# Optimization experiments

Measured on AMD Instinct MI355X. Metric: run time of the kernel, lower is better.

Reference implementation:

```python
import jax, jax.numpy as jnp
import numpy as np

N_NODES = 80000
N_EDGES = 1280000
D_NODE = 128
D_EDGE = 32
HID = 64
OUT = 32
EPS_GEN = 1e-7
EPS_BN = 1e-5


def _lin_init(key, fan_in, fan_out):
    return (jax.random.normal(key, (fan_in, fan_out), jnp.float32) / np.sqrt(fan_in))


def setup_inputs() -> dict:
    key = jax.random.key(0)
    ks = jax.random.split(key, 20)
    inp = {
        "x": jax.random.normal(ks[0], (N_NODES, D_NODE), jnp.float32),
        "edge_index": jax.random.randint(ks[1], (2, N_EDGES), 0, N_NODES, jnp.int32),
        "edge_attr": jax.random.normal(ks[2], (N_EDGES, D_EDGE), jnp.float32),
        # encoders
        "node_W": _lin_init(ks[3], D_NODE, HID), "node_b": jnp.zeros((HID,), jnp.float32),
        "edge_W": _lin_init(ks[4], D_EDGE, HID), "edge_b": jnp.zeros((HID,), jnp.float32),
        # GENConv layer 1 MLP: [HID -> 2HID (bias=False)] -> BN -> ReLU -> [2HID -> HID (bias=False)]
        "c1_W1": _lin_init(ks[5], HID, 2 * HID), "c1_g": jnp.ones((2 * HID,), jnp.float32), "c1_be": jnp.zeros((2 * HID,), jnp.float32), "c1_W2": _lin_init(ks[6], 2 * HID, HID),
        # GENConv layer 2
        "c2_W1": _lin_init(ks[7], HID, 2 * HID), "c2_g": jnp.ones((2 * HID,), jnp.float32), "c2_be": jnp.zeros((2 * HID,), jnp.float32), "c2_W2": _lin_init(ks[8], 2 * HID, HID),
        # edge update linears on concat(3*HID)
        "l1_W": _lin_init(ks[9], 3 * HID, HID), "l1_b": jnp.zeros((HID,), jnp.float32),
        "l2_W": _lin_init(ks[10], 3 * HID, OUT), "l2_b": jnp.zeros((OUT,), jnp.float32),
    }
    return inp


def _scatter_softmax_agg(msg, dst, n_nodes):
    # SoftmaxAggregation with t=1: per-destination, per-feature softmax weights
    m = jax.ops.segment_max(msg, dst, num_segments=n_nodes)  # [N, H]
    m = jnp.where(jnp.isfinite(m), m, 0.0)                   # nodes w/o in-edges
    ex = jnp.exp(msg - m[dst])                               # [E, H]
    denom = jax.ops.segment_sum(ex, dst, num_segments=n_nodes)
    alpha = ex / (denom[dst] + 1e-16)
    return jax.ops.segment_sum(msg * alpha, dst, num_segments=n_nodes)


def _batchnorm(h, gamma, beta):
    mu = jnp.mean(h, axis=0)
    var = jnp.var(h, axis=0)
    return (h - mu) * jax.lax.rsqrt(var + EPS_BN) * gamma + beta


def _genconv(x, src, dst, edge_attr, W1, g, be, W2):
    msg = jax.nn.relu(x[src] + edge_attr) + EPS_GEN          # [E, HID]
    agg = _scatter_softmax_agg(msg, dst, x.shape[0])         # [N, HID]
    h = agg + x
    h = jax.nn.relu(_batchnorm(h @ W1, g, be))
    return h @ W2


def reference(x, edge_index, edge_attr, node_W, node_b, edge_W, edge_b,
              c1_W1, c1_g, c1_be, c1_W2, c2_W1, c2_g, c2_be, c2_W2,
              l1_W, l1_b, l2_W, l2_b):
    src, dst = edge_index[0], edge_index[1]
    ea = edge_attr @ edge_W + edge_b                          # [E, HID]
    h = x @ node_W + node_b                                   # [N, HID]

    convs = [(c1_W1, c1_g, c1_be, c1_W2), (c2_W1, c2_g, c2_be, c2_W2)]
    lins = [(l1_W, l1_b), (l2_W, l2_b)]
    for (W1, g, be, W2), (lW, lb) in zip(convs, lins):
        h = jax.nn.relu(_genconv(h, src, dst, ea, W1, g, be, W2))
        # dropout is identity in eval mode
        ef = jnp.concatenate([h[src], ea, h[dst]], axis=-1)   # [E, 3*HID]
        ea = ef @ lW + lb
    return h, ea
```

## Files before the change

### kernel.cpp

```cpp
#include <hip/hip_runtime.h>
#include <hip/hip_bf16.h>

#define N_NODES 80000
#define N_EDGES 1280000
constexpr int DN = 128;
constexpr int DE = 32;
constexpr int H  = 64;
constexpr int H2 = 128;
constexpr int CSTRIDE = 32;
constexpr float EPS_GEN = 1e-7f;
constexpr float EPS_BN  = 1e-5f;

typedef _Float16 f16x8 __attribute__((ext_vector_type(8)));
typedef _Float16 f16x4 __attribute__((ext_vector_type(4)));
typedef float f32x4 __attribute__((ext_vector_type(4)));

__device__ __forceinline__ void atomAddF(float* p, float v) {
  __hip_atomic_fetch_add(p, v, __ATOMIC_RELAXED, __HIP_MEMORY_SCOPE_AGENT);
}

struct PrepDesc { const float* W; _Float16* img; int K; int OC; int blkStart; };
struct PrepAll { PrepDesc d[8]; };

__global__ void k_prep_all(PrepAll P) {
  int b = blockIdx.x;
  int i = 0;
#pragma unroll
  for (int t = 1; t < 8; ++t)
    if (P.d[t].blkStart <= b) i = t;
  const PrepDesc D = P.d[i];
  int idx = (b - D.blkStart) * 256 + threadIdx.x;
  if (idx >= D.K * D.OC) return;
  int nslabK = D.K >> 5;
  int j = idx & 7, m16 = (idx >> 3) & 15, kg = (idx >> 7) & 3;
  int slab = idx >> 9;
  int kk = slab % nslabK, n2 = slab / nslabK;
  int k = kk * 32 + kg * 8 + j, n = n2 * 16 + m16;
  D.img[idx] = (_Float16)D.W[k * D.OC + n];
}

template <int K, int OC, bool IN16, bool BIAS,
          bool RELU_OUT, bool OUT16, bool OUT32, bool SCATOUT, bool STATS>
__global__ __launch_bounds__(256) void k_dense(
    const void* __restrict__ Ain, const _Float16* __restrict__ wimg,
    const float* __restrict__ bias,
    const int* __restrict__ posmap,
    _Float16* __restrict__ out16, float* __restrict__ out32,
    float* __restrict__ sums_out) {
  constexpr int NK = K / 32, NF = OC / 16;
  __shared__ float sStat[STATS ? 1024 : 1];
  const int tid = threadIdx.x, wv = tid >> 6, lane = tid & 63;
  const int m16 = lane & 15, kg = lane >> 4;
  const int rowbase = blockIdx.x * 64 + wv * 16;
  const int arow = rowbase + m16;
  f32x4 acc[NF];
#pragma unroll
  for (int n2 = 0; n2 < NF; ++n2) {
    float bv = BIAS ? bias[n2 * 16 + m16] : 0.0f;
    acc[n2] = (f32x4){bv, bv, bv, bv};
  }
  const _Float16* wp = wimg + (size_t)lane * 8;
#pragma unroll
  for (int kk = 0; kk < NK; ++kk) {
    f16x8 a;
    if constexpr (IN16) {
      const _Float16* ap = (const _Float16*)Ain + (size_t)arow * K + kg * 8 + kk * 32;
      a = *(const f16x8*)ap;
    } else {
      const float* ap = (const float*)Ain + (size_t)arow * K + kg * 8 + kk * 32;
      float4 v0 = *(const float4*)ap;
      float4 v1 = *(const float4*)(ap + 4);
      a = (f16x8){(_Float16)v0.x, (_Float16)v0.y, (_Float16)v0.z, (_Float16)v0.w,
                  (_Float16)v1.x, (_Float16)v1.y, (_Float16)v1.z, (_Float16)v1.w};
    }
#pragma unroll
    for (int n2 = 0; n2 < NF; ++n2) {
      f16x8 bb = *(const f16x8*)(wp + ((size_t)(n2 * NK + kk) << 9));
      acc[n2] = __builtin_amdgcn_mfma_f32_16x16x32_f16(a, bb, acc[n2], 0, 0, 0);
    }
  }
  if constexpr (OUT16 || OUT32) {
#pragma unroll
    for (int n2 = 0; n2 < NF; ++n2)
#pragma unroll
      for (int r = 0; r < 4; ++r) {
        float o = acc[n2][r];
        if constexpr (RELU_OUT) o = fmaxf(o, 0.0f);
        int orow = rowbase + kg * 4 + r;
        if constexpr (SCATOUT) orow = posmap[orow];
        size_t oi = (size_t)orow * OC + n2 * 16 + m16;
        if constexpr (OUT16) out16[oi] = (_Float16)o;
        if constexpr (OUT32) out32[oi] = o;
      }
  }
  if constexpr (STATS) {
    static_assert(!STATS || NF == 8, "STATS assumes OC==128");
#pragma unroll
    for (int n2 = 0; n2 < NF; ++n2) {
      float s = acc[n2][0] + acc[n2][1] + acc[n2][2] + acc[n2][3];
      float q = acc[n2][0] * acc[n2][0] + acc[n2][1] * acc[n2][1] +
                acc[n2][2] * acc[n2][2] + acc[n2][3] * acc[n2][3];
      s += __shfl_xor(s, 16); s += __shfl_xor(s, 32);
      q += __shfl_xor(q, 16); q += __shfl_xor(q, 32);
      if (kg == 0) {
        sStat[wv * 128 + n2 * 16 + m16] = s;
        sStat[512 + wv * 128 + n2 * 16 + m16] = q;
      }
    }
    __syncthreads();
    {
      int which = tid >> 7, f = tid & 127;
      const float* b0 = sStat + which * 512;
      float v = b0[f] + b0[128 + f] + b0[256 + f] + b0[384 + f];
      atomAddF(&sums_out[which * H2 + f], v);
    }
  }
}

template <bool OUT32>
__global__ __launch_bounds__(256) void k_mlp2f(
    const _Float16* __restrict__ hsum, const _Float16* __restrict__ w1img,
    const _Float16* __restrict__ w2img, const float* __restrict__ sums,
    const float* __restrict__ g, const float* __restrict__ be,
    _Float16* __restrict__ out16, float* __restrict__ out32) {
  constexpr int TP = 136;
  __shared__ float sSC[H2], sSH[H2];
  __shared__ _Float16 sT[64 * TP];
  const int tid = threadIdx.x, wv = tid >> 6, lane = tid & 63;
  const int m16 = lane & 15, kg = lane >> 4;
  const int rowbase = blockIdx.x * 64 + wv * 16;

  for (int i = tid; i < H2; i += 256) {
    float mu  = sums[i] * (1.0f / N_NODES);
    float var = sums[H2 + i] * (1.0f / N_NODES) - mu * mu;
    float sc  = rsqrtf(var + EPS_BN) * g[i];
    sSC[i] = sc;
    sSH[i] = be[i] - mu * sc;
  }

  f32x4 acc1[8];
#pragma unroll
  for (int n2 = 0; n2 < 8; ++n2) acc1[n2] = (f32x4){0.f, 0.f, 0.f, 0.f};
  const _Float16* wp1 = w1img + (size_t)lane * 8;
#pragma unroll
  for (int kk = 0; kk < 2; ++kk) {
    f16x8 a = *(const f16x8*)(hsum + (size_t)(rowbase + m16) * H + kg * 8 + kk * 32);
#pragma unroll
    for (int n2 = 0; n2 < 8; ++n2) {
      f16x8 bb = *(const f16x8*)(wp1 + ((size_t)(n2 * 2 + kk) << 9));
      acc1[n2] = __builtin_amdgcn_mfma_f32_16x16x32_f16(a, bb, acc1[n2], 0, 0, 0);
    }
  }
  __syncthreads();
#pragma unroll
  for (int n2 = 0; n2 < 8; ++n2) {
    int col = n2 * 16 + m16;
    float sc = sSC[col], sh = sSH[col];
#pragma unroll
    for (int r = 0; r < 4; ++r) {
      float v = fmaxf(fmaf(acc1[n2][r], sc, sh), 0.0f);
      sT[(wv * 16 + kg * 4 + r) * TP + col] = (_Float16)v;
    }
  }
  __syncthreads();
  f32x4 acc2[4];
#pragma unroll
  for (int n2 = 0; n2 < 4; ++n2) acc2[n2] = (f32x4){0.f, 0.f, 0.f, 0.f};
  const _Float16* wp2 = w2img + (size_t)lane * 8;
#pragma unroll
  for (int kk = 0; kk < 4; ++kk) {
    f16x8 a2 = *(const f16x8*)&sT[(wv * 16 + m16) * TP + kg * 8 + kk * 32];
#pragma unroll
    for (int n2 = 0; n2 < 4; ++n2) {
      f16x8 bb = *(const f16x8*)(wp2 + ((size_t)(n2 * 4 + kk) << 9));
      acc2[n2] = __builtin_amdgcn_mfma_f32_16x16x32_f16(a2, bb, acc2[n2], 0, 0, 0);
    }
  }
#pragma unroll
  for (int n2 = 0; n2 < 4; ++n2)
#pragma unroll
    for (int r = 0; r < 4; ++r) {
      float o = fmaxf(acc2[n2][r], 0.0f);
      size_t oi = (size_t)(rowbase + kg * 4 + r) * H + n2 * 16 + m16;
      out16[oi] = (_Float16)o;
      if constexpr (OUT32) out32[oi] = o;
    }
}

template <int OC, typename OUT_T, int T, bool SCAT>
__global__ __launch_bounds__(256) void k_edge_upd_srt(
    const _Float16* __restrict__ h, const _Float16* __restrict__ ea,
    const int4* __restrict__ eidsQ,
    const _Float16* __restrict__ wimg, const float* __restrict__ lb,
    OUT_T* __restrict__ eout) {
  constexpr int NF = OC / 16;
  __shared__ _Float16 sWf[NF * 6 * 512];
  __shared__ int sS[T * 64], sD[T * 64];
  __shared__ int sE[SCAT ? T * 64 : 1];
  const int tid = threadIdx.x, wv = tid >> 6, lane = tid & 63;
  const int m16 = lane & 15, kg = lane >> 4;
  const int p0 = blockIdx.x * (T * 64);

  for (int i = tid; i < T * 64; i += 256) {
    int4 t = eidsQ[p0 + i];
    sS[i] = t.y;
    sD[i] = t.z;
    if constexpr (SCAT) sE[i] = t.x;
  }
  {
    const float4* s4 = (const float4*)wimg;
    float4* d4 = (float4*)sWf;
    constexpr int NV = NF * 6 * 512 / 8;
    for (int i = tid; i < NV; i += 256) d4[i] = s4[i];
  }
  __syncthreads();
  const _Float16* wp = sWf + (size_t)lane * 8;

  float bias_[NF];
#pragma unroll
  for (int n2 = 0; n2 < NF; ++n2) bias_[n2] = lb[n2 * 16 + m16];

  f16x8 FA[6], FB[6];
  auto LOADA = [&](f16x8* F, int l) {
    const _Float16* a0 = h + (size_t)sS[l] * H + kg * 8;
    const _Float16* a1 = ea + (size_t)(p0 + l) * H + kg * 8;
    const _Float16* a2 = h + (size_t)sD[l] * H + kg * 8;
    F[0] = *(const f16x8*)a0;
    F[1] = *(const f16x8*)(a0 + 32);
    F[2] = *(const f16x8*)a1;
    F[3] = *(const f16x8*)(a1 + 32);
    F[4] = *(const f16x8*)a2;
    F[5] = *(const f16x8*)(a2 + 32);
  };
  auto COMPUTE = [&](const f16x8* F, int l) {
    f32x4 acc[NF];
#pragma unroll
    for (int n2 = 0; n2 < NF; ++n2)
      acc[n2] = (f32x4){bias_[n2], bias_[n2], bias_[n2], bias_[n2]};
#pragma unroll
    for (int kk = 0; kk < 6; ++kk)
#pragma unroll
      for (int n2 = 0; n2 < NF; ++n2) {
        f16x8 bb = *(const f16x8*)(wp + ((n2 * 6 + kk) << 9));
        acc[n2] = __builtin_amdgcn_mfma_f32_16x16x32_f16(F[kk], bb, acc[n2], 0, 0, 0);
      }
    const int lbase = l - m16;
#pragma unroll
    for (int n2 = 0; n2 < NF; ++n2)
#pragma unroll
      for (int r = 0; r < 4; ++r) {
        int lr = lbase + kg * 4 + r;
        int col = n2 * 16 + m16;
        if constexpr (SCAT)
          eout[(size_t)sE[lr] * OC + col] = (OUT_T)acc[n2][r];
        else
          eout[(size_t)(p0 + lr) * OC + col] = (OUT_T)acc[n2][r];
      }
  };

  const int l0 = wv * 16 + m16;
  LOADA(FA, l0);
  if (T > 1) LOADA(FB, l0 + 64);
#pragma unroll
  for (int t = 0; t < T; ++t) {
    if (t & 1) {
      COMPUTE(FB, l0 + t * 64);
      if (t + 2 < T) LOADA(FB, l0 + (t + 2) * 64);
    } else {
      COMPUTE(FA, l0 + t * 64);
      if (t + 2 < T) LOADA(FA, l0 + (t + 2) * 64);
    }
  }
}

__global__ void k_rank(const int* __restrict__ dst, int* cntPad, int* __restrict__ rank) {
  int e = blockIdx.x * blockDim.x + threadIdx.x;
  if (e < N_EDGES)
    rank[e] = atomicAdd(&cntPad[(size_t)dst[e] * CSTRIDE], 1);
}

__global__ void k_scan_blk(const int* __restrict__ cntPad, int* __restrict__ bsum) {
  __shared__ int sh[256];
  int i = blockIdx.x * 256 + threadIdx.x;
  sh[threadIdx.x] = (i < N_NODES) ? cntPad[(size_t)i * CSTRIDE] : 0;
  __syncthreads();
  for (int s = 128; s > 0; s >>= 1) {
    if (threadIdx.x < s) sh[threadIdx.x] += sh[threadIdx.x + s];
    __syncthreads();
  }
  if (threadIdx.x == 0) bsum[blockIdx.x] = sh[0];
}

__global__ void k_scan_top(int* bsum, int nb) {
  __shared__ int sh[512];
  int t = threadIdx.x;
  int orig = (t < nb) ? bsum[t] : 0;
  sh[t] = orig;
  __syncthreads();
  for (int off = 1; off < 512; off <<= 1) {
    int v = (t >= off) ? sh[t - off] : 0;
    __syncthreads();
    sh[t] += v;
    __syncthreads();
  }
  if (t < nb) bsum[t] = sh[t] - orig;
}

__global__ void k_scan_fin(const int* __restrict__ cntPad, const int* __restrict__ bsum,
                           int* __restrict__ start, int* __restrict__ cntC) {
  __shared__ int sh[256];
  int i = blockIdx.x * 256 + threadIdx.x;
  int t = threadIdx.x;
  int orig = (i < N_NODES) ? cntPad[(size_t)i * CSTRIDE] : 0;
  sh[t] = orig;
  __syncthreads();
  for (int off = 1; off < 256; off <<= 1) {
    int v = (t >= off) ? sh[t - off] : 0;
    __syncthreads();
    sh[t] += v;
    __syncthreads();
  }
  if (i < N_NODES) {
    start[i] = bsum[blockIdx.x] + sh[t] - orig;
    cntC[i] = orig;
  }
}

__global__ void k_scatter(const int* __restrict__ src, const int* __restrict__ dst,
                          const int* __restrict__ rank, const int* __restrict__ start,
                          int4* __restrict__ eidsQ, int* __restrict__ posOf) {
  int e = blockIdx.x * blockDim.x + threadIdx.x;
  if (e < N_EDGES) {
    int d = dst[e];
    int pos = start[d] + rank[e];
    eidsQ[pos] = make_int4(e, src[e], d, 0);
    posOf[e] = pos;
  }
}

__global__ __launch_bounds__(256) void k_agg_csr(
    const _Float16* __restrict__ h, const _Float16* __restrict__ ea_s,
    const int4* __restrict__ eidsQ, const int* __restrict__ start,
    const int* __restrict__ cnt, _Float16* __restrict__ hsum,
    float* __restrict__ sums_clr) {
  if (blockIdx.x == 0) sums_clr[threadIdx.x] = 0.0f;
  const int lane = threadIdx.x & 63;
  const int wid  = (int)((blockIdx.x * blockDim.x + threadIdx.x) >> 6);
  if (wid >= N_NODES) return;
  const int ep = lane >> 3, fg = lane & 7;
  const int s0 = start[wid], c = cnt[wid];
  float num[8] = {0.f, 0.f, 0.f, 0.f, 0.f, 0.f, 0.f, 0.f};
  float den[8] = {0.f, 0.f, 0.f, 0.f, 0.f, 0.f, 0.f, 0.f};
  if (c > 0) {
    const int nit = (c + 7) >> 3;
    int idx = min(ep, c - 1);
    int2 pe = *(const int2*)(eidsQ + s0 + idx);
    f16x8 hA = *(const f16x8*)(h + (size_t)pe.y * H + fg * 8);
    f16x8 eA = *(const f16x8*)(ea_s + (size_t)(s0 + idx) * H + fg * 8);
    bool vA = (ep < c);
    f16x8 hB = hA, eB = eA;
    bool vB = false;
    if (nit > 1) {
      idx = min(8 + ep, c - 1);
      pe = *(const int2*)(eidsQ + s0 + idx);
      hB = *(const f16x8*)(h + (size_t)pe.y * H + fg * 8);
      eB = *(const f16x8*)(ea_s + (size_t)(s0 + idx) * H + fg * 8);
      vB = (8 + ep < c);
    }
    for (int i = 0; i < nit; ++i) {
      f16x8 hc = hA, ec = eA;
      bool vc = vA;
      hA = hB; eA = eB; vA = vB;
      if (i + 2 < nit) {
        idx = min((i + 2) * 8 + ep, c - 1);
        pe = *(const int2*)(eidsQ + s0 + idx);
        hB = *(const f16x8*)(h + (size_t)pe.y * H + fg * 8);
        eB = *(const f16x8*)(ea_s + (size_t)(s0 + idx) * H + fg * 8);
        vB = ((i + 2) * 8 + ep < c);
      }
#pragma unroll
      for (int j = 0; j < 8; ++j) {
        float m = fmaxf((float)hc[j] + (float)ec[j], 0.0f) + EPS_GEN;
        float ex = vc ? __expf(m) : 0.0f;
        num[j] = fmaf(m, ex, num[j]);
        den[j] += ex;
      }
    }
  }
#pragma unroll
  for (int j = 0; j < 8; ++j) {
    num[j] += __shfl_xor(num[j], 8);
    num[j] += __shfl_xor(num[j], 16);
    num[j] += __shfl_xor(num[j], 32);
    den[j] += __shfl_xor(den[j], 8);
    den[j] += __shfl_xor(den[j], 16);
    den[j] += __shfl_xor(den[j], 32);
  }
  if (ep == 0) {
    f16x8 hs = *(const f16x8*)(h + (size_t)wid * H + fg * 8);
    f16x8 o;
#pragma unroll
    for (int j = 0; j < 8; ++j)
      o[j] = (_Float16)(num[j] / (den[j] + 1e-16f) + (float)hs[j]);
    *(f16x8*)(hsum + (size_t)wid * H + fg * 8) = o;
  }
}

extern "C" void kernel_launch(void* const* d_in, const int* in_sizes, int n_in,
                              void* d_out, int out_size, void* d_ws, size_t ws_size,
                              hipStream_t stream) {
  (void)in_sizes; (void)n_in; (void)out_size; (void)ws_size;
  const float* x      = (const float*)d_in[0];
  const int*   eidx   = (const int*)d_in[1];
  const float* eattr  = (const float*)d_in[2];
  const float* node_W = (const float*)d_in[3];
  const float* node_b = (const float*)d_in[4];
  const float* edge_W = (const float*)d_in[5];
  const float* edge_b = (const float*)d_in[6];
  const float* c1_W1  = (const float*)d_in[7];
  const float* c1_g   = (const float*)d_in[8];
  const float* c1_be  = (const float*)d_in[9];
  const float* c1_W2  = (const float*)d_in[10];
  const float* c2_W1  = (const float*)d_in[11];
  const float* c2_g   = (const float*)d_in[12];
  const float* c2_be  = (const float*)d_in[13];
  const float* c2_W2  = (const float*)d_in[14];
  const float* l1_W   = (const float*)d_in[15];
  const float* l1_b   = (const float*)d_in[16];
  const float* l2_W   = (const float*)d_in[17];
  const float* l2_b   = (const float*)d_in[18];

  const int* src = eidx;
  const int* dst = eidx + N_EDGES;

  char* wsb = (char*)d_ws;
  size_t off = 0;
  _Float16* ea_s  = (_Float16*)(wsb + off); off += (size_t)N_EDGES * H * 2;
  _Float16* hA16  = (_Float16*)(wsb + off); off += (size_t)N_NODES * H * 2;
  _Float16* hB16  = (_Float16*)(wsb + off); off += (size_t)N_NODES * H * 2;
  _Float16* hC16  = (_Float16*)(wsb + off); off += (size_t)N_NODES * H * 2;
  _Float16* hsum16= (_Float16*)(wsb + off); off += (size_t)N_NODES * H * 2;
  float* sums     = (float*)(wsb + off);    off += 256 * 4;
  int* cntPad     = (int*)(wsb + off);      off += (size_t)N_NODES * CSTRIDE * 4;
  int* startA     = (int*)(wsb + off);      off += (size_t)N_NODES * 4;
  int* cntC       = (int*)(wsb + off);      off += (size_t)N_NODES * 4;
  int* bsum       = (int*)(wsb + off);      off += 512 * 4;
  int* rankE      = (int*)(wsb + off);      off += (size_t)N_EDGES * 4;
  int4* eidsQ     = (int4*)(wsb + off);     off += (size_t)N_EDGES * 16;
  int* posOf      = (int*)(wsb + off);      off += (size_t)N_EDGES * 4;
  _Float16* wE    = (_Float16*)(wsb + off); off += DE * H * 2;
  _Float16* wN    = (_Float16*)(wsb + off); off += DN * H * 2;
  _Float16* w1a   = (_Float16*)(wsb + off); off += H * H2 * 2;
  _Float16* w1b   = (_Float16*)(wsb + off); off += H * H2 * 2;
  _Float16* w2a   = (_Float16*)(wsb + off); off += H2 * H * 2;
  _Float16* w2b   = (_Float16*)(wsb + off); off += H2 * H * 2;
  _Float16* wL1   = (_Float16*)(wsb + off); off += 3 * H * H * 2;
  _Float16* wL2   = (_Float16*)(wsb + off); off += 3 * H * 32 * 2;

  float* h_out  = (float*)d_out;
  float* ea_out = (float*)d_out + (size_t)N_NODES * H;

  constexpr int NB = (N_NODES + 255) / 256;

  PrepAll P;
  P.d[0] = {edge_W, wE, DE, H, 0};
  P.d[1] = {node_W, wN, DN, H, 8};
  P.d[2] = {c1_W1, w1a, H, H2, 40};
  P.d[3] = {c2_W1, w1b, H, H2, 72};
  P.d[4] = {c1_W2, w2a, H2, H, 104};
  P.d[5] = {c2_W2, w2b, H2, H, 136};
  P.d[6] = {l1_W, wL1, 192, H, 168};
  P.d[7] = {l2_W, wL2, 192, 32, 216};
  k_prep_all<<<240, 256, 0, stream>>>(P);

  hipMemsetAsync(cntPad, 0, (size_t)N_NODES * CSTRIDE * 4, stream);
  k_rank<<<(N_EDGES + 255) / 256, 256, 0, stream>>>(dst, cntPad, rankE);
  k_scan_blk<<<NB, 256, 0, stream>>>(cntPad, bsum);
  k_scan_top<<<1, 512, 0, stream>>>(bsum, NB);
  k_scan_fin<<<NB, 256, 0, stream>>>(cntPad, bsum, startA, cntC);
  k_scatter<<<(N_EDGES + 255) / 256, 256, 0, stream>>>(src, dst, rankE, startA, eidsQ, posOf);

  k_dense<DE, H, false, true, false, true, false, true, false>
      <<<N_EDGES / 64, 256, 0, stream>>>(eattr, wE, edge_b,
                                         posOf, ea_s, nullptr, nullptr);
  k_dense<DN, H, false, true, false, true, false, false, false>
      <<<N_NODES / 64, 256, 0, stream>>>(x, wN, node_b,
                                         nullptr, hA16, nullptr, nullptr);

  k_agg_csr<<<(N_NODES + 3) / 4, 256, 0, stream>>>(hA16, ea_s, eidsQ, startA, cntC, hsum16, sums);
  k_dense<H, H2, true, false, false, false, false, false, true>
      <<<N_NODES / 64, 256, 0, stream>>>(hsum16, w1a, nullptr,
                                         nullptr, nullptr, nullptr, sums);
  k_mlp2f<false><<<N_NODES / 64, 256, 0, stream>>>(hsum16, w1a, w2a, sums,
                                                   c1_g, c1_be, hB16, nullptr);
  k_edge_upd_srt<64, _Float16, 16, false>
      <<<N_EDGES / 1024, 256, 0, stream>>>(hB16, ea_s, eidsQ, wL1, l1_b, ea_s);

  k_agg_csr<<<(N_NODES + 3) / 4, 256, 0, stream>>>(hB16, ea_s, eidsQ, startA, cntC, hsum16, sums);
  k_dense<H, H2, true, false, false, false, false, false, true>
      <<<N_NODES / 64, 256, 0, stream>>>(hsum16, w1b, nullptr,
                                         nullptr, nullptr, nullptr, sums);
  k_mlp2f<true><<<N_NODES / 64, 256, 0, stream>>>(hsum16, w1b, w2b, sums,
                                                  c2_g, c2_be, hC16, h_out);
  k_edge_upd_srt<32, float, 16, true>
      <<<N_EDGES / 1024, 256, 0, stream>>>(hC16, ea_s, eidsQ, wL2, l2_b, ea_out);
}
```

Before: 594.1 us.

## Widen per-lane edge slots in CSR aggregation and fold memset into prep kernel

The softmax aggregation kernel now assigns 16 edges per wavefront iteration, with each lane covering 16 features in two 8-wide loads instead of 8 edges by 8 features. This halves loop iterations per node and gives more independent loads in flight, at the cost of more registers and a longer shuffle reduction. Separately, the hipMemsetAsync of the count buffer is replaced by extra blocks appended to the weight-prep kernel that zero it, removing one launch or memset call.

```diff
diff --git a/kernel.cpp b/kernel.cpp
--- a/kernel.cpp
+++ b/kernel.cpp
@@ -20,10 +20,15 @@
 }
 
 struct PrepDesc { const float* W; _Float16* img; int K; int OC; int blkStart; };
-struct PrepAll { PrepDesc d[8]; };
+struct PrepAll { PrepDesc d[8]; float4* zero; int prepBlocks; size_t zeroN; };
 
 __global__ void k_prep_all(PrepAll P) {
   int b = blockIdx.x;
+  if (b >= P.prepBlocks) {
+    size_t i = (size_t)(b - P.prepBlocks) * 256 + threadIdx.x;
+    if (i < P.zeroN) P.zero[i] = (float4){0.f, 0.f, 0.f, 0.f};
+    return;
+  }
   int i = 0;
 #pragma unroll
   for (int t = 1; t < 8; ++t)
@@ -347,62 +352,67 @@
   const int lane = threadIdx.x & 63;
   const int wid  = (int)((blockIdx.x * blockDim.x + threadIdx.x) >> 6);
   if (wid >= N_NODES) return;
-  const int ep = lane >> 3, fg = lane & 7;
+  const int ep = lane & 15, fg = lane >> 4;
   const int s0 = start[wid], c = cnt[wid];
-  float num[8] = {0.f, 0.f, 0.f, 0.f, 0.f, 0.f, 0.f, 0.f};
-  float den[8] = {0.f, 0.f, 0.f, 0.f, 0.f, 0.f, 0.f, 0.f};
+  float num[16], den[16];
+#pragma unroll
+  for (int j = 0; j < 16; ++j) { num[j] = 0.0f; den[j] = 0.0f; }
   if (c > 0) {
-    const int nit = (c + 7) >> 3;
-    int idx = min(ep, c - 1);
-    int2 pe = *(const int2*)(eidsQ + s0 + idx);
-    f16x8 hA = *(const f16x8*)(h + (size_t)pe.y * H + fg * 8);
-    f16x8 eA = *(const f16x8*)(ea_s + (size_t)(s0 + idx) * H + fg * 8);
-    bool vA = (ep < c);
-    f16x8 hB = hA, eB = eA;
-    bool vB = false;
-    if (nit > 1) {
-      idx = min(8 + ep, c - 1);
-      pe = *(const int2*)(eidsQ + s0 + idx);
-      hB = *(const f16x8*)(h + (size_t)pe.y * H + fg * 8);
-      eB = *(const f16x8*)(ea_s + (size_t)(s0 + idx) * H + fg * 8);
-      vB = (8 + ep < c);
-    }
+    const int nit = (c + 15) >> 4;
+    auto LD = [&](int i, f16x8& h0, f16x8& h1, f16x8& e0, f16x8& e1, bool& v) {
+      int idx = min(i * 16 + ep, c - 1);
+      int2 pe = *(const int2*)(eidsQ + s0 + idx);
+      const _Float16* hp = h + (size_t)pe.y * H + fg * 16;
+      const _Float16* eap = ea_s + (size_t)(s0 + idx) * H + fg * 16;
+      h0 = *(const f16x8*)hp;  h1 = *(const f16x8*)(hp + 8);
+      e0 = *(const f16x8*)eap; e1 = *(const f16x8*)(eap + 8);
+      v = (i * 16 + ep < c);
+    };
+    f16x8 hA0, hA1, eA0, eA1, hB0, hB1, eB0, eB1;
+    bool vA = false, vB = false;
+    LD(0, hA0, hA1, eA0, eA1, vA);
+    if (nit > 1) LD(1, hB0, hB1, eB0, eB1, vB);
     for (int i = 0; i < nit; ++i) {
-      f16x8 hc = hA, ec = eA;
+      f16x8 h0 = hA0, h1 = hA1, e0 = eA0, e1 = eA1;
       bool vc = vA;
-      hA = hB; eA = eB; vA = vB;
-      if (i + 2 < nit) {
-        idx = min((i + 2) * 8 + ep, c - 1);
-        pe = *(const int2*)(eidsQ + s0 + idx);
-        hB = *(const f16x8*)(h + (size_t)pe.y * H + fg * 8);
-        eB = *(const f16x8*)(ea_s + (size_t)(s0 + idx) * H + fg * 8);
-        vB = ((i + 2) * 8 + ep < c);
+      hA0 = hB0; hA1 = hB1; eA0 = eB0; eA1 = eB1; vA = vB;
+      if (i + 2 < nit) LD(i + 2, hB0, hB1, eB0, eB1, vB);
+#pragma unroll
+      for (int j = 0; j < 8; ++j) {
+        float m0 = fmaxf((float)h0[j] + (float)e0[j], 0.0f) + EPS_GEN;
+        float x0 = vc ? __expf(m0) : 0.0f;
+        num[j] = fmaf(m0, x0, num[j]);
+        den[j] += x0;
+        float m1 = fmaxf((float)h1[j] + (float)e1[j], 0.0f) + EPS_GEN;
+        float x1 = vc ? __expf(m1) : 0.0f;
+        num[8 + j] = fmaf(m1, x1, num[8 + j]);
+        den[8 + j] += x1;
       }
-#pragma unroll
-      for (int j = 0; j < 8; ++j) {
-        float m = fmaxf((float)hc[j] + (float)ec[j], 0.0f) + EPS_GEN;
-        float ex = vc ? __expf(m) : 0.0f;
-        num[j] = fmaf(m, ex, num[j]);
-        den[j] += ex;
-      }
-    }
-  }
-#pragma unroll
-  for (int j = 0; j < 8; ++j) {
+    }
+  }
+#pragma unroll
+  for (int j = 0; j < 16; ++j) {
+    num[j] += __shfl_xor(num[j], 1);
+    num[j] += __shfl_xor(num[j], 2);
+    num[j] += __shfl_xor(num[j], 4);
     num[j] += __shfl_xor(num[j], 8);
-    num[j] += __shfl_xor(num[j], 16);
-    num[j] += __shfl_xor(num[j], 32);
+    den[j] += __shfl_xor(den[j], 1);
+    den[j] += __shfl_xor(den[j], 2);
+    den[j] += __shfl_xor(den[j], 4);
     den[j] += __shfl_xor(den[j], 8);
-    den[j] += __shfl_xor(den[j], 16);
-    den[j] += __shfl_xor(den[j], 32);
   }
   if (ep == 0) {
-    f16x8 hs = *(const f16x8*)(h + (size_t)wid * H + fg * 8);
-    f16x8 o;
-#pragma unroll
-    for (int j = 0; j < 8; ++j)
-      o[j] = (_Float16)(num[j] / (den[j] + 1e-16f) + (float)hs[j]);
-    *(f16x8*)(hsum + (size_t)wid * H + fg * 8) = o;
+    const _Float16* hp = h + (size_t)wid * H + fg * 16;
+    f16x8 hs0 = *(const f16x8*)hp, hs1 = *(const f16x8*)(hp + 8);
+    f16x8 o0, o1;
+#pragma unroll
+    for (int j = 0; j < 8; ++j) {
+      o0[j] = (_Float16)(num[j] / (den[j] + 1e-16f) + (float)hs0[j]);
+      o1[j] = (_Float16)(num[8 + j] / (den[8 + j] + 1e-16f) + (float)hs1[j]);
+    }
+    _Float16* op = hsum + (size_t)wid * H + fg * 16;
+    *(f16x8*)op = o0;
+    *(f16x8*)(op + 8) = o1;
   }
 }
 
@@ -471,9 +481,11 @@
   P.d[5] = {c2_W2, w2b, H2, H, 136};
   P.d[6] = {l1_W, wL1, 192, H, 168};
   P.d[7] = {l2_W, wL2, 192, 32, 216};
-  k_prep_all<<<240, 256, 0, stream>>>(P);
-
-  hipMemsetAsync(cntPad, 0, (size_t)N_NODES * CSTRIDE * 4, stream);
+  P.zero = (float4*)cntPad;
+  P.prepBlocks = 240;
+  P.zeroN = (size_t)N_NODES * CSTRIDE / 4;
+  k_prep_all<<<240 + 2500, 256, 0, stream>>>(P);
+
   k_rank<<<(N_EDGES + 255) / 256, 256, 0, stream>>>(dst, cntPad, rankE);
   k_scan_blk<<<NB, 256, 0, stream>>>(cntPad, bsum);
   k_scan_top<<<1, 512, 0, stream>>>(bsum, NB);
```

Result: slower. 711.3 us (+19.7%).
